# Optimization experiments

Measured on AMD Instinct MI355X. Metric: run time of the kernel, lower is better.

The kernel has to match this reference:

```python
import jax, jax.numpy as jnp
import numpy as np

SPARSITY_PROB = 0.1
CAUSAL = True
B, H, S, D = 2, 16, 2048, 64


def _make_mask(key, seq_len, sparsity_prob, causal):
    # random_mask = rand < p, optionally AND causal tril, then force diagonal True
    m = jax.random.uniform(key, (seq_len, seq_len)) < sparsity_prob
    if causal:
        m = m & jnp.tril(jnp.ones((seq_len, seq_len), dtype=bool))
    idx = jnp.arange(seq_len)
    m = m.at[idx, idx].set(True)
    return m


def setup_inputs() -> dict:
    key = jax.random.key(0)
    kq, kk, kv, km = jax.random.split(key, 4)
    query = jax.random.normal(kq, (B, H, S, D), dtype=jnp.float32)
    k_ = jax.random.normal(kk, (B, H, S, D), dtype=jnp.float32)
    v_ = jax.random.normal(kv, (B, H, S, D), dtype=jnp.float32)
    mask = _make_mask(km, S, SPARSITY_PROB, CAUSAL)
    return {"query": query, "key": k_, "value": v_, "mask": mask}


def reference(query, key, value, mask):
    # Masked attention: softmax over the selected positions of each row is
    # mathematically identical to the per-row gather+softmax in the original.
    # mask: [S, S] bool, shared across batch and heads; every row has at least
    # the diagonal True, so no fully-masked rows.
    head_dim = query.shape[-1]
    scale = 1.0 / jnp.sqrt(jnp.asarray(head_dim, dtype=query.dtype))
    scores = jnp.einsum("bhqd,bhkd->bhqk", query, key) * scale  # [B,H,S,S]
    scores = jnp.where(mask[None, None, :, :], scores, -jnp.inf)
    attn = jax.nn.softmax(scores, axis=-1)
    return jnp.einsum("bhqk,bhkd->bhqd", attn, value)
```

## Files before the change

kernel.cpp:

```cpp
#include <hip/hip_runtime.h>
#include <hip/hip_bf16.h>

#define SEQ 2048
#define HD 64
#define NBH 32
#define SCALE 0.125f
#define QSC 0.18033688011112042f

typedef __attribute__((ext_vector_type(4)))  float    f32x4;
typedef __attribute__((ext_vector_type(16))) float    f32x16;
typedef __attribute__((ext_vector_type(8)))  short    bf16x8;
typedef __attribute__((ext_vector_type(4)))  unsigned u32x4;

__device__ inline short f2bf(float f) {
    unsigned u = __builtin_bit_cast(unsigned, f);
    unsigned r = u + 0x7FFFu + ((u >> 16) & 1u);
    return (short)(r >> 16);
}

__device__ inline unsigned cvt2(float lo, float hi) {
    unsigned d;
    asm("v_cvt_pk_bf16_f32 %0, %1, %2" : "=v"(d) : "v"(lo), "v"(hi));
    return d;
}

__global__ void detect_mask_kernel(const unsigned char* __restrict__ m, int n, int* flag) {
    if (threadIdx.x == 0) *flag = (m[n - 1] != 0) ? 1 : 4;
}

__global__ __launch_bounds__(256)
void prep_kernel(const unsigned char* __restrict__ m, const int* __restrict__ flag,
                 const float* __restrict__ K, const float* __restrict__ V,
                 unsigned* __restrict__ bits, short* __restrict__ Kb,
                 short* __restrict__ Vt) {
    __shared__ short t[64][65];
    const int b = blockIdx.x, tid = threadIdx.x;
    if (b < 512) {
        const int idx = b * 256 + tid;
        const int row = idx >> 6, w = idx & 63;
        const size_t base = (size_t)row * SEQ + w * 32;
        unsigned word = 0;
        if (*flag == 1) {
            #pragma unroll
            for (int i = 0; i < 32; ++i) word |= (unsigned)(m[base + i] != 0) << i;
        } else {
            const unsigned* m32 = (const unsigned*)m;
            #pragma unroll
            for (int i = 0; i < 32; ++i) word |= (unsigned)(m32[base + i] != 0) << i;
        }
        bits[(size_t)w * SEQ + row] = word;
    } else if (b < 2560) {
        const int g = (b - 512) * 256 + tid;
        const size_t i = (size_t)g * 8;
        f32x4 a = *(const f32x4*)(K + i);
        f32x4 c = *(const f32x4*)(K + i + 4);
        bf16x8 o;
        #pragma unroll
        for (int j = 0; j < 4; ++j) { o[j] = f2bf(a[j]); o[4 + j] = f2bf(c[j]); }
        const int row = g >> 3;
        const int c8  = g & 7;
        const int bh  = row >> 11;
        const int r   = row & 2047;
        const int tt  = r >> 5;
        const int la  = r & 31;
        *(bf16x8*)(Kb + ((size_t)bh * 64 + tt) * 2048 + (c8 * 32 + la) * 8) = o;
    } else {
        const int bb = b - 2560;
        const int s0 = (bb & 31) * 64, bh = bb >> 5;
        const float* Vb = V + (size_t)bh * SEQ * HD;
        const int sr = tid >> 6, d = tid & 63;
        #pragma unroll
        for (int i = 0; i < 16; ++i) {
            const int s = i * 4 + sr;
            t[s][d] = f2bf(Vb[(size_t)(s0 + s) * HD + d]);
        }
        __syncthreads();
        short* o = Vt + (size_t)bh * HD * SEQ;
        const int dr = tid >> 6, sl = tid & 63;
        #pragma unroll
        for (int i = 0; i < 16; ++i) {
            const int dd = i * 4 + dr;
            const int s = s0 + sl;
            const int k = s & 31;
            const int p = (k & ~12) | ((k & 8) >> 1) | ((k & 4) << 1);
            const int mm = ((dd >> 5) << 1) | (p >> 4);
            const int hh = (p >> 3) & 1;
            o[(size_t)(s >> 5) * 2048 + ((mm * 2 + hh) * 32 + (dd & 31)) * 8 + (p & 7)] = t[sl][dd];
        }
    }
}

__global__ __launch_bounds__(256, 2)
void attn_shared_kernel(const float* __restrict__ Q, const short* __restrict__ Kb,
                        const short* __restrict__ Vt, const unsigned* __restrict__ bitsT,
                        float* __restrict__ Out) {
    __shared__ __align__(16) short kbuf[2][2048];
    __shared__ __align__(16) short vbuf[2][2048];
    __shared__ short oacc[4][32][72];

    const int id   = blockIdx.x;
    const int bh   = id & 31;
    const int qg   = 15 - (id >> 5);
    const int tid  = threadIdx.x;
    const int wid  = tid >> 6;
    const int lane = tid & 63;
    const int la   = lane & 31;
    const int h    = lane >> 5;
    const int q0w  = qg * 128 + wid * 32;
    const int nt   = qg * 4 + 4;
    const size_t base = (size_t)bh * SEQ * HD;

    bf16x8 qf[4];
    {
        const float* qp = Q + base + (size_t)(q0w + la) * HD + h * 8;
        #pragma unroll
        for (int j = 0; j < 4; ++j) {
            f32x4 a0 = *(const f32x4*)(qp + j * 16);
            f32x4 a1 = *(const f32x4*)(qp + j * 16 + 4);
            #pragma unroll
            for (int i = 0; i < 4; ++i) {
                qf[j][i]     = f2bf(a0[i] * QSC);
                qf[j][4 + i] = f2bf(a1[i] * QSC);
            }
        }
    }

    f32x16 acc_o0 = {0,0,0,0,0,0,0,0,0,0,0,0,0,0,0,0};
    f32x16 acc_o1 = {0,0,0,0,0,0,0,0,0,0,0,0,0,0,0,0};
    float l_run = 0.f;

    const short* Ktg = Kb + (size_t)bh * 64 * 2048;
    const short* Vtg = Vt + (size_t)bh * 64 * 2048;
    const unsigned* bq = bitsT + q0w + la;
    const int bp = 4 * h;

    {
        bf16x8 sk = *(const bf16x8*)(Ktg + (size_t)tid * 8);
        bf16x8 sv = *(const bf16x8*)(Vtg + (size_t)tid * 8);
        *(bf16x8*)(&kbuf[0][0] + tid * 8) = sk;
        *(bf16x8*)(&vbuf[0][0] + tid * 8) = sv;
    }
    unsigned mw = bq[0];

    int cur = 0;
    for (int t = 0; t < nt; ++t) {
        __syncthreads();

        const short* kb = &kbuf[cur][0];
        const short* vb = &vbuf[cur][0];
        bf16x8 kfa = *(const bf16x8*)(kb + lane * 8);
        bf16x8 kfb = *(const bf16x8*)(kb + 512 + lane * 8);
        bf16x8 kfc = *(const bf16x8*)(kb + 1024 + lane * 8);
        bf16x8 kfd = *(const bf16x8*)(kb + 1536 + lane * 8);
        bf16x8 vf00 = *(const bf16x8*)(vb + lane * 8);
        bf16x8 vf01 = *(const bf16x8*)(vb + 512 + lane * 8);
        bf16x8 vf10 = *(const bf16x8*)(vb + 1024 + lane * 8);
        bf16x8 vf11 = *(const bf16x8*)(vb + 1536 + lane * 8);

        const int tn = (t + 1 < nt) ? t + 1 : t;
        bf16x8 sk = *(const bf16x8*)(Ktg + (size_t)tn * 2048 + tid * 8);
        bf16x8 sv = *(const bf16x8*)(Vtg + (size_t)tn * 2048 + tid * 8);
        unsigned nmw = bq[(size_t)tn * SEQ];

        f32x16 sA = {0,0,0,0,0,0,0,0,0,0,0,0,0,0,0,0};
        f32x16 sB = {0,0,0,0,0,0,0,0,0,0,0,0,0,0,0,0};
        __builtin_amdgcn_s_setprio(1);
        sA = __builtin_amdgcn_mfma_f32_32x32x16_bf16(kfa, qf[0], sA, 0, 0, 0);
        sB = __builtin_amdgcn_mfma_f32_32x32x16_bf16(kfc, qf[2], sB, 0, 0, 0);
        sA = __builtin_amdgcn_mfma_f32_32x32x16_bf16(kfb, qf[1], sA, 0, 0, 0);
        sB = __builtin_amdgcn_mfma_f32_32x32x16_bf16(kfd, qf[3], sB, 0, 0, 0);
        __builtin_amdgcn_s_setprio(0);
        f32x16 s = sA + sB;

        #pragma unroll
        for (int r = 0; r < 16; ++r) {
            float e = __builtin_amdgcn_exp2f(s[r]);
            s[r] = ((mw >> (bp + (r & 3) + 8 * (r >> 2))) & 1u) ? e : 0.f;
        }
        float ps = ((s[0] + s[1]) + (s[2] + s[3])) + ((s[4] + s[5]) + (s[6] + s[7]));
        ps += ((s[8] + s[9]) + (s[10] + s[11])) + ((s[12] + s[13]) + (s[14] + s[15]));
        l_run += ps;

        u32x4 t1 = {cvt2(s[0], s[1]),  cvt2(s[2], s[3]),
                    cvt2(s[4], s[5]),  cvt2(s[6], s[7])};
        u32x4 t2 = {cvt2(s[8], s[9]),  cvt2(s[10], s[11]),
                    cvt2(s[12], s[13]), cvt2(s[14], s[15])};
        bf16x8 pb1 = __builtin_bit_cast(bf16x8, t1);
        bf16x8 pb2 = __builtin_bit_cast(bf16x8, t2);

        __builtin_amdgcn_s_setprio(1);
        acc_o0 = __builtin_amdgcn_mfma_f32_32x32x16_bf16(vf00, pb1, acc_o0, 0, 0, 0);
        acc_o1 = __builtin_amdgcn_mfma_f32_32x32x16_bf16(vf10, pb1, acc_o1, 0, 0, 0);
        acc_o0 = __builtin_amdgcn_mfma_f32_32x32x16_bf16(vf01, pb2, acc_o0, 0, 0, 0);
        acc_o1 = __builtin_amdgcn_mfma_f32_32x32x16_bf16(vf11, pb2, acc_o1, 0, 0, 0);
        __builtin_amdgcn_s_setprio(0);

        *(bf16x8*)(&kbuf[cur ^ 1][0] + tid * 8) = sk;
        *(bf16x8*)(&vbuf[cur ^ 1][0] + tid * 8) = sv;

        mw = nmw;
        cur ^= 1;
    }

    {
        const float l_full = l_run + __shfl_xor(l_run, 32);
        const float invw = 1.f / l_full;
        unsigned short* orow = (unsigned short*)&oacc[wid][la][0];
        #pragma unroll
        for (int g = 0; g < 4; ++g) {
            const int d0 = 8 * g + 4 * h;
            unsigned w0 = cvt2(acc_o0[4 * g + 0] * invw, acc_o0[4 * g + 1] * invw);
            unsigned w1 = cvt2(acc_o0[4 * g + 2] * invw, acc_o0[4 * g + 3] * invw);
            unsigned w2 = cvt2(acc_o1[4 * g + 0] * invw, acc_o1[4 * g + 1] * invw);
            unsigned w3 = cvt2(acc_o1[4 * g + 2] * invw, acc_o1[4 * g + 3] * invw);
            *(unsigned*)&orow[d0]      = w0;
            *(unsigned*)&orow[d0 + 2]  = w1;
            *(unsigned*)&orow[d0 + 32] = w2;
            *(unsigned*)&orow[d0 + 34] = w3;
        }
    }
    __syncthreads();

    {
        const int q  = tid >> 3;
        const int dc = (tid & 7) * 8;
        #pragma unroll
        for (int k = 0; k < 4; ++k) {
            u32x4 pk = *(const u32x4*)&oacc[k][q][dc];
            float o[8];
            #pragma unroll
            for (int j = 0; j < 4; ++j) {
                o[2 * j]     = __builtin_bit_cast(float, (pk[j] & 0xFFFFu) << 16);
                o[2 * j + 1] = __builtin_bit_cast(float, pk[j] & 0xFFFF0000u);
            }
            float* op = Out + base + (size_t)(qg * 128 + k * 32 + q) * HD + dc;
            f32x4 o0v = {o[0], o[1], o[2], o[3]};
            f32x4 o1v = {o[4], o[5], o[6], o[7]};
            *(f32x4*)op       = o0v;
            *(f32x4*)(op + 4) = o1v;
        }
    }
}

__global__ __launch_bounds__(256)
void attn_kernel(const float* __restrict__ Q, const float* __restrict__ K,
                 const float* __restrict__ V, const unsigned char* __restrict__ mask,
                 const int* __restrict__ flag, float* __restrict__ Out) {
    __shared__ short plds[4][16][40];
    const int esz  = *flag;
    const int bh   = blockIdx.y;
    const int wid  = threadIdx.x >> 6;
    const int lane = threadIdx.x & 63;
    const int l16  = lane & 15;
    const int hi   = lane >> 4;
    const int q0   = blockIdx.x * 64 + wid * 16;
    const size_t base = (size_t)bh * SEQ * HD;
    const float* Qb = Q + base;
    const float* Kb = K + base;
    const float* Vb = V + base;
    const unsigned int* mask32 = (const unsigned int*)mask;
    bf16x8 qf[2];
    {
        const float* qp = Qb + (size_t)(q0 + l16) * HD + hi * 8;
        f32x4 a0 = *(const f32x4*)(qp);
        f32x4 a1 = *(const f32x4*)(qp + 4);
        f32x4 a2 = *(const f32x4*)(qp + 32);
        f32x4 a3 = *(const f32x4*)(qp + 36);
        #pragma unroll
        for (int i = 0; i < 4; ++i) {
            qf[0][i] = f2bf(a0[i]); qf[0][4 + i] = f2bf(a1[i]);
            qf[1][i] = f2bf(a2[i]); qf[1][4 + i] = f2bf(a3[i]);
        }
    }
    f32x4 acc_o[4] = {f32x4{0,0,0,0}, f32x4{0,0,0,0}, f32x4{0,0,0,0}, f32x4{0,0,0,0}};
    float m_run[4], l_run[4];
    #pragma unroll
    for (int j = 0; j < 4; ++j) { m_run[j] = -__builtin_inff(); l_run[j] = 0.f; }
    const int kv_end = q0 + 16;
    for (int kv = 0; kv < kv_end; kv += 32) {
        f32x4 acc_s[2] = {f32x4{0,0,0,0}, f32x4{0,0,0,0}};
        #pragma unroll
        for (int t = 0; t < 2; ++t) {
            const float* kp = Kb + (size_t)(kv + 16 * t + l16) * HD + hi * 8;
            f32x4 b0 = *(const f32x4*)(kp);
            f32x4 b1 = *(const f32x4*)(kp + 4);
            f32x4 b2 = *(const f32x4*)(kp + 32);
            f32x4 b3 = *(const f32x4*)(kp + 36);
            bf16x8 kf0, kf1;
            #pragma unroll
            for (int i = 0; i < 4; ++i) {
                kf0[i] = f2bf(b0[i]); kf0[4 + i] = f2bf(b1[i]);
                kf1[i] = f2bf(b2[i]); kf1[4 + i] = f2bf(b3[i]);
            }
            acc_s[t] = __builtin_amdgcn_mfma_f32_16x16x32_bf16(qf[0], kf0, acc_s[t], 0, 0, 0);
            acc_s[t] = __builtin_amdgcn_mfma_f32_16x16x32_bf16(qf[1], kf1, acc_s[t], 0, 0, 0);
        }
        float s[2][4];
        #pragma unroll
        for (int t = 0; t < 2; ++t) {
            const int k = kv + 16 * t + l16;
            #pragma unroll
            for (int j = 0; j < 4; ++j) {
                const int qrow = q0 + hi * 4 + j;
                const size_t midx = (size_t)qrow * SEQ + k;
                const bool mv = (esz == 1) ? (mask[midx] != 0) : (mask32[midx] != 0);
                s[t][j] = mv ? acc_s[t][j] * SCALE : -__builtin_inff();
            }
        }
        float mnew[4], r[4];
        #pragma unroll
        for (int j = 0; j < 4; ++j) {
            float v = fmaxf(s[0][j], s[1][j]);
            #pragma unroll
            for (int off = 1; off < 16; off <<= 1) v = fmaxf(v, __shfl_xor(v, off));
            mnew[j] = fmaxf(m_run[j], v);
            r[j] = (m_run[j] > -__builtin_inff()) ? __expf(m_run[j] - mnew[j]) : 0.f;
        }
        float p[2][4];
        #pragma unroll
        for (int j = 0; j < 4; ++j) {
            float ps = 0.f;
            #pragma unroll
            for (int t = 0; t < 2; ++t) {
                p[t][j] = (s[t][j] > -__builtin_inff()) ? __expf(s[t][j] - mnew[j]) : 0.f;
                ps += p[t][j];
            }
            #pragma unroll
            for (int off = 1; off < 16; off <<= 1) ps += __shfl_xor(ps, off);
            l_run[j] = l_run[j] * r[j] + ps;
            m_run[j] = mnew[j];
            #pragma unroll
            for (int t2 = 0; t2 < 4; ++t2) acc_o[t2][j] *= r[j];
        }
        #pragma unroll
        for (int t = 0; t < 2; ++t)
            #pragma unroll
            for (int j = 0; j < 4; ++j)
                plds[wid][hi * 4 + j][16 * t + l16] = f2bf(p[t][j]);
        bf16x8 pa = *(bf16x8*)&plds[wid][l16][hi * 8];
        #pragma unroll
        for (int t2 = 0; t2 < 4; ++t2) {
            const float* vp = Vb + (size_t)(kv + hi * 8) * HD + 16 * t2 + l16;
            bf16x8 vf;
            #pragma unroll
            for (int i = 0; i < 8; ++i) vf[i] = f2bf(vp[(size_t)i * HD]);
            acc_o[t2] = __builtin_amdgcn_mfma_f32_16x16x32_bf16(pa, vf, acc_o[t2], 0, 0, 0);
        }
    }
    #pragma unroll
    for (int j = 0; j < 4; ++j) {
        const float inv = 1.f / l_run[j];
        const int qrow = q0 + hi * 4 + j;
        float* op = Out + base + (size_t)qrow * HD + l16;
        #pragma unroll
        for (int t2 = 0; t2 < 4; ++t2) op[16 * t2] = acc_o[t2][j] * inv;
    }
}

extern "C" void kernel_launch(void* const* d_in, const int* in_sizes, int n_in,
                              void* d_out, int out_size, void* d_ws, size_t ws_size,
                              hipStream_t stream) {
    const float* Q = (const float*)d_in[0];
    const float* K = (const float*)d_in[1];
    const float* V = (const float*)d_in[2];
    const unsigned char* mask = (const unsigned char*)d_in[3];

    const size_t bitsB = (size_t)SEQ * (SEQ / 32) * 4;
    const size_t kvB   = (size_t)NBH * SEQ * HD * 2;
    const size_t need  = bitsB + 2 * kvB + 256;

    if (ws_size >= need) {
        unsigned* bits = (unsigned*)d_ws;
        short* Kb = (short*)((char*)d_ws + bitsB);
        short* Vt = (short*)((char*)d_ws + bitsB + kvB);
        int* flag = (int*)((char*)d_ws + bitsB + 2 * kvB);

        detect_mask_kernel<<<dim3(1), dim3(64), 0, stream>>>(mask, in_sizes[3], flag);
        prep_kernel<<<dim3(3584), dim3(256), 0, stream>>>(mask, flag, K, V, bits, Kb, Vt);
        attn_shared_kernel<<<dim3(512), dim3(256), 0, stream>>>(Q, Kb, Vt, bits, (float*)d_out);
    } else {
        int* flag = (int*)d_ws;
        detect_mask_kernel<<<dim3(1), dim3(64), 0, stream>>>(mask, in_sizes[3], flag);
        attn_kernel<<<dim3(SEQ / 64, NBH), dim3(256), 0, stream>>>(Q, K, V, mask, flag, (float*)d_out);
    }
}
```

Baseline: 62.39 us.

## Drop LDS K/V staging and barriers, fold mask detection into prep, reorder blocks

Removes the shared-memory double buffer for K/V tiles so each wave loads its own fragments straight from global memory into registers with a one-tile prefetch. This eliminates the per-iteration __syncthreads. The separate detect-mask kernel launch is removed and each prep block reads the mask's last element itself. The block-to-query-group mapping changes so the second half of the grid runs heavy groups in ascending order. The cost is four times more global/L2 traffic for K/V, because each of the 4 waves loads the same tile, plus higher register pressure. The QK MFMAs are also now one dependent chain instead of two interleaved ones.

```diff
diff --git a/kernel.cpp b/kernel.cpp
--- a/kernel.cpp
+++ b/kernel.cpp
@@ -29,18 +29,19 @@
 }
 
 __global__ __launch_bounds__(256)
-void prep_kernel(const unsigned char* __restrict__ m, const int* __restrict__ flag,
+void prep_kernel(const unsigned char* __restrict__ m, int mn,
                  const float* __restrict__ K, const float* __restrict__ V,
                  unsigned* __restrict__ bits, short* __restrict__ Kb,
                  short* __restrict__ Vt) {
     __shared__ short t[64][65];
     const int b = blockIdx.x, tid = threadIdx.x;
     if (b < 512) {
+        const bool e1 = (m[mn - 1] != 0);
         const int idx = b * 256 + tid;
         const int row = idx >> 6, w = idx & 63;
         const size_t base = (size_t)row * SEQ + w * 32;
         unsigned word = 0;
-        if (*flag == 1) {
+        if (e1) {
             #pragma unroll
             for (int i = 0; i < 32; ++i) word |= (unsigned)(m[base + i] != 0) << i;
         } else {
@@ -91,16 +92,14 @@
 }
 
 __global__ __launch_bounds__(256, 2)
-void attn_shared_kernel(const float* __restrict__ Q, const short* __restrict__ Kb,
-                        const short* __restrict__ Vt, const unsigned* __restrict__ bitsT,
-                        float* __restrict__ Out) {
-    __shared__ __align__(16) short kbuf[2][2048];
-    __shared__ __align__(16) short vbuf[2][2048];
+void attn_nobar_kernel(const float* __restrict__ Q, const short* __restrict__ Kb,
+                       const short* __restrict__ Vt, const unsigned* __restrict__ bitsT,
+                       float* __restrict__ Out) {
     __shared__ short oacc[4][32][72];
 
     const int id   = blockIdx.x;
     const int bh   = id & 31;
-    const int qg   = 15 - (id >> 5);
+    const int qg   = (id < 256) ? (15 - (id >> 5)) : ((id - 256) >> 5);
     const int tid  = threadIdx.x;
     const int wid  = tid >> 6;
     const int lane = tid & 63;
@@ -129,53 +128,24 @@
     f32x16 acc_o1 = {0,0,0,0,0,0,0,0,0,0,0,0,0,0,0,0};
     float l_run = 0.f;
 
-    const short* Ktg = Kb + (size_t)bh * 64 * 2048;
-    const short* Vtg = Vt + (size_t)bh * 64 * 2048;
+    const short* Ktg = Kb + (size_t)bh * 64 * 2048 + lane * 8;
+    const short* Vtg = Vt + (size_t)bh * 64 * 2048 + lane * 8;
     const unsigned* bq = bitsT + q0w + la;
     const int bp = 4 * h;
 
-    {
-        bf16x8 sk = *(const bf16x8*)(Ktg + (size_t)tid * 8);
-        bf16x8 sv = *(const bf16x8*)(Vtg + (size_t)tid * 8);
-        *(bf16x8*)(&kbuf[0][0] + tid * 8) = sk;
-        *(bf16x8*)(&vbuf[0][0] + tid * 8) = sv;
-    }
-    unsigned mw = bq[0];
-
-    int cur = 0;
-    for (int t = 0; t < nt; ++t) {
-        __syncthreads();
-
-        const short* kb = &kbuf[cur][0];
-        const short* vb = &vbuf[cur][0];
-        bf16x8 kfa = *(const bf16x8*)(kb + lane * 8);
-        bf16x8 kfb = *(const bf16x8*)(kb + 512 + lane * 8);
-        bf16x8 kfc = *(const bf16x8*)(kb + 1024 + lane * 8);
-        bf16x8 kfd = *(const bf16x8*)(kb + 1536 + lane * 8);
-        bf16x8 vf00 = *(const bf16x8*)(vb + lane * 8);
-        bf16x8 vf01 = *(const bf16x8*)(vb + 512 + lane * 8);
-        bf16x8 vf10 = *(const bf16x8*)(vb + 1024 + lane * 8);
-        bf16x8 vf11 = *(const bf16x8*)(vb + 1536 + lane * 8);
-
-        const int tn = (t + 1 < nt) ? t + 1 : t;
-        bf16x8 sk = *(const bf16x8*)(Ktg + (size_t)tn * 2048 + tid * 8);
-        bf16x8 sv = *(const bf16x8*)(Vtg + (size_t)tn * 2048 + tid * 8);
-        unsigned nmw = bq[(size_t)tn * SEQ];
-
-        f32x16 sA = {0,0,0,0,0,0,0,0,0,0,0,0,0,0,0,0};
-        f32x16 sB = {0,0,0,0,0,0,0,0,0,0,0,0,0,0,0,0};
+    auto body = [&](const bf16x8* kf, const bf16x8* vf, unsigned mwx) {
+        f32x16 s = {0,0,0,0,0,0,0,0,0,0,0,0,0,0,0,0};
         __builtin_amdgcn_s_setprio(1);
-        sA = __builtin_amdgcn_mfma_f32_32x32x16_bf16(kfa, qf[0], sA, 0, 0, 0);
-        sB = __builtin_amdgcn_mfma_f32_32x32x16_bf16(kfc, qf[2], sB, 0, 0, 0);
-        sA = __builtin_amdgcn_mfma_f32_32x32x16_bf16(kfb, qf[1], sA, 0, 0, 0);
-        sB = __builtin_amdgcn_mfma_f32_32x32x16_bf16(kfd, qf[3], sB, 0, 0, 0);
+        s = __builtin_amdgcn_mfma_f32_32x32x16_bf16(kf[0], qf[0], s, 0, 0, 0);
+        s = __builtin_amdgcn_mfma_f32_32x32x16_bf16(kf[1], qf[1], s, 0, 0, 0);
+        s = __builtin_amdgcn_mfma_f32_32x32x16_bf16(kf[2], qf[2], s, 0, 0, 0);
+        s = __builtin_amdgcn_mfma_f32_32x32x16_bf16(kf[3], qf[3], s, 0, 0, 0);
         __builtin_amdgcn_s_setprio(0);
-        f32x16 s = sA + sB;
 
         #pragma unroll
         for (int r = 0; r < 16; ++r) {
             float e = __builtin_amdgcn_exp2f(s[r]);
-            s[r] = ((mw >> (bp + (r & 3) + 8 * (r >> 2))) & 1u) ? e : 0.f;
+            s[r] = ((mwx >> (bp + (r & 3) + 8 * (r >> 2))) & 1u) ? e : 0.f;
         }
         float ps = ((s[0] + s[1]) + (s[2] + s[3])) + ((s[4] + s[5]) + (s[6] + s[7]));
         ps += ((s[8] + s[9]) + (s[10] + s[11])) + ((s[12] + s[13]) + (s[14] + s[15]));
@@ -189,22 +159,41 @@
         bf16x8 pb2 = __builtin_bit_cast(bf16x8, t2);
 
         __builtin_amdgcn_s_setprio(1);
-        acc_o0 = __builtin_amdgcn_mfma_f32_32x32x16_bf16(vf00, pb1, acc_o0, 0, 0, 0);
-        acc_o1 = __builtin_amdgcn_mfma_f32_32x32x16_bf16(vf10, pb1, acc_o1, 0, 0, 0);
-        acc_o0 = __builtin_amdgcn_mfma_f32_32x32x16_bf16(vf01, pb2, acc_o0, 0, 0, 0);
-        acc_o1 = __builtin_amdgcn_mfma_f32_32x32x16_bf16(vf11, pb2, acc_o1, 0, 0, 0);
+        acc_o0 = __builtin_amdgcn_mfma_f32_32x32x16_bf16(vf[0], pb1, acc_o0, 0, 0, 0);
+        acc_o1 = __builtin_amdgcn_mfma_f32_32x32x16_bf16(vf[2], pb1, acc_o1, 0, 0, 0);
+        acc_o0 = __builtin_amdgcn_mfma_f32_32x32x16_bf16(vf[1], pb2, acc_o0, 0, 0, 0);
+        acc_o1 = __builtin_amdgcn_mfma_f32_32x32x16_bf16(vf[3], pb2, acc_o1, 0, 0, 0);
         __builtin_amdgcn_s_setprio(0);
-
-        *(bf16x8*)(&kbuf[cur ^ 1][0] + tid * 8) = sk;
-        *(bf16x8*)(&vbuf[cur ^ 1][0] + tid * 8) = sv;
-
+    };
+
+    bf16x8 kf[4], vf[4], nk[4], nv[4];
+    #pragma unroll
+    for (int j = 0; j < 4; ++j) {
+        kf[j] = *(const bf16x8*)(Ktg + j * 512);
+        vf[j] = *(const bf16x8*)(Vtg + j * 512);
+    }
+    unsigned mw = bq[0];
+
+    for (int t = 0; t < nt; ++t) {
+        const int tn = (t + 1 < nt) ? t + 1 : t;
+        #pragma unroll
+        for (int j = 0; j < 4; ++j) {
+            nk[j] = *(const bf16x8*)(Ktg + (size_t)tn * 2048 + j * 512);
+            nv[j] = *(const bf16x8*)(Vtg + (size_t)tn * 2048 + j * 512);
+        }
+        unsigned nmw = bq[(size_t)tn * SEQ];
+
+        body(kf, vf, mw);
+
+        #pragma unroll
+        for (int j = 0; j < 4; ++j) { kf[j] = nk[j]; vf[j] = nv[j]; }
         mw = nmw;
-        cur ^= 1;
-    }
+    }
+
+    const float l_full = l_run + __shfl_xor(l_run, 32);
+    const float invw = 1.f / l_full;
 
     {
-        const float l_full = l_run + __shfl_xor(l_run, 32);
-        const float invw = 1.f / l_full;
         unsigned short* orow = (unsigned short*)&oacc[wid][la][0];
         #pragma unroll
         for (int g = 0; g < 4; ++g) {
@@ -373,11 +362,9 @@
         unsigned* bits = (unsigned*)d_ws;
         short* Kb = (short*)((char*)d_ws + bitsB);
         short* Vt = (short*)((char*)d_ws + bitsB + kvB);
-        int* flag = (int*)((char*)d_ws + bitsB + 2 * kvB);
-
-        detect_mask_kernel<<<dim3(1), dim3(64), 0, stream>>>(mask, in_sizes[3], flag);
-        prep_kernel<<<dim3(3584), dim3(256), 0, stream>>>(mask, flag, K, V, bits, Kb, Vt);
-        attn_shared_kernel<<<dim3(512), dim3(256), 0, stream>>>(Q, Kb, Vt, bits, (float*)d_out);
+
+        prep_kernel<<<dim3(3584), dim3(256), 0, stream>>>(mask, in_sizes[3], K, V, bits, Kb, Vt);
+        attn_nobar_kernel<<<dim3(512), dim3(256), 0, stream>>>(Q, Kb, Vt, bits, (float*)d_out);
     } else {
         int* flag = (int*)d_ws;
         detect_mask_kernel<<<dim3(1), dim3(64), 0, stream>>>(mask, in_sizes[3], flag);
```

New measurement: 57.36 us. 1.09x faster.
